# Kernel tuning notes

Measured on AMD Instinct MI355X. Metric: run time of the kernel, lower is better.

## Reference

```python
import jax, jax.numpy as jnp
import numpy as np

B, U, D_DEC, D_ENC = 32, 4096, 512, 512
ATT_UNITS, NUM_HEADS = 512, 4
HEAD_DIM = ATT_UNITS // NUM_HEADS
CONV_FILTERS, CONV_K = 32, 31
INIT = 0.075


def setup_inputs() -> dict:
    key = jax.random.key(0)
    ks = jax.random.split(key, 12)
    u = lambda k, shape: jax.random.uniform(k, shape, jnp.float32, -INIT, INIT)
    return {
        "dec_state": jax.random.normal(ks[0], (B, D_DEC), jnp.float32),
        "enc_state": jax.random.normal(ks[1], (B, U, D_ENC), jnp.float32),
        "prev_attention_weights": jax.random.uniform(ks[2], (B, U), jnp.float32),
        # stacked per-head Dense params
        "Wphi": u(ks[3], (NUM_HEADS, D_DEC, HEAD_DIM)),
        "bphi": jnp.zeros((NUM_HEADS, HEAD_DIM), jnp.float32),
        "Wpsi": u(ks[4], (NUM_HEADS, D_ENC, HEAD_DIM)),
        "bpsi": jnp.zeros((NUM_HEADS, HEAD_DIM), jnp.float32),
        # Conv1D kernel in WIO layout: (kernel_size, in_ch=1, out_ch=32), no bias
        "conv_kernel": jax.random.uniform(ks[5], (CONV_K, 1, CONV_FILTERS), jnp.float32, -0.1, 0.1),
        "Wloc": u(ks[6], (CONV_FILTERS, NUM_HEADS)),
        "Wout": u(ks[7], (NUM_HEADS * D_ENC, ATT_UNITS)),
        "bout": jnp.zeros((ATT_UNITS,), jnp.float32),
    }


def reference(dec_state, enc_state, prev_attention_weights,
              Wphi, bphi, Wpsi, bpsi, conv_kernel, Wloc, Wout, bout):
    # location features: Conv1D(same, no bias) over prev attention weights
    loc_feat = jax.lax.conv_general_dilated(
        prev_attention_weights[:, :, None], conv_kernel,
        window_strides=(1,), padding="SAME",
        dimension_numbers=("NWC", "WIO", "NWC"))            # (B, U, 32)
    loc_bias = loc_feat @ Wloc                                 # (B, U, H)
    loc_bias = jnp.transpose(loc_bias, (0, 2, 1))              # (B, H, U)

    # batched per-head projections (replaces the Python per-head loop)
    phi_s = jnp.einsum("bd,hdk->bhk", dec_state, Wphi) + bphi          # (B, H, hd)
    psi_h = jnp.einsum("bue,hek->bhuk", enc_state, Wpsi) + bpsi[:, None, :]  # (B, H, U, hd)

    energy = jnp.einsum("bhk,bhuk->bhu", phi_s, psi_h) + loc_bias      # (B, H, U)
    attn = jax.nn.softmax(energy, axis=-1)                              # (B, H, U)

    context = jnp.einsum("bhu,bue->bhe", attn, enc_state)               # (B, H, E)
    combined = context.reshape(context.shape[0], -1)                    # (B, H*E)
    context_vector = combined @ Wout + bout                             # (B, ATT_UNITS)
    attention_weights = jnp.mean(attn, axis=1)                          # (B, U)
    return context_vector, attention_weights
```

## Files before the change

kernel.cpp:

```cpp
#include <hip/hip_runtime.h>
#include <math.h>

#define B  32
#define U  4096
#define D  512
#define H  4
#define HD 128
#define CK 31
#define CF 32
#define AU 512

#define WPB    128
#define ROWS_W 32

__global__ __launch_bounds__(256) void prep_kernel(
    const float* __restrict__ dec,
    const float* __restrict__ Wphi,
    const float* __restrict__ bphi,
    const float* __restrict__ Wpsi,
    const float* __restrict__ bpsi,
    const float* __restrict__ convk,
    const float* __restrict__ Wloc,
    float* __restrict__ ws_v,
    float* __restrict__ ws_const,
    float* __restrict__ ws_ck)
{
    __shared__ float decs[D];
    __shared__ float phis[HD];
    const int b = blockIdx.x / H, h = blockIdx.x % H;
    const int tid = threadIdx.x;

    for (int i = tid; i < D; i += 256) decs[i] = dec[b * D + i];
    __syncthreads();

    if (tid < HD) {
        float acc = bphi[h * HD + tid];
        const float* wp = Wphi + (size_t)h * D * HD + tid;
        #pragma unroll 8
        for (int d = 0; d < D; ++d) acc += decs[d] * wp[(size_t)d * HD];
        phis[tid] = acc;
    }
    __syncthreads();

    if (tid == 0) {
        float c = 0.f;
        for (int k = 0; k < HD; ++k) c += phis[k] * bpsi[h * HD + k];
        ws_const[b * H + h] = c;
    }

    for (int e = tid; e < D; e += 256) {
        const float* wq = Wpsi + ((size_t)h * D + e) * HD;
        float acc = 0.f;
        #pragma unroll 8
        for (int k = 0; k < HD; ++k) acc += wq[k] * phis[k];
        ws_v[((size_t)b * H + h) * D + e] = acc;
    }

    if (blockIdx.x == 0 && tid < CK * H) {
        int t = tid / H, hh = tid % H;
        float acc = 0.f;
        for (int f = 0; f < CF; ++f) acc += convk[t * CF + f] * Wloc[f * H + hh];
        ws_ck[t * H + hh] = acc;
    }
}

__global__ __launch_bounds__(256) void fused_pass1(
    const float* __restrict__ enc,
    const float* __restrict__ prevw,
    const float* __restrict__ ws_v,
    const float* __restrict__ ws_const,
    const float* __restrict__ ws_ck,
    float* __restrict__ energy,
    float* __restrict__ pctx,
    float* __restrict__ pms)
{
    const int b    = blockIdx.y;
    const int tid  = threadIdx.x;
    const int lane = tid & 63;
    const int wave = tid >> 6;
    const int widx = blockIdx.x * 4 + wave;
    const int ubase = widx * ROWS_W;

    float4 v0[H], v1[H];
    #pragma unroll
    for (int h = 0; h < H; ++h) {
        const float* vp = ws_v + ((size_t)b * H + h) * D + lane * 8;
        v0[h] = *(const float4*)vp;
        v1[h] = *(const float4*)(vp + 4);
    }
    float ckr[H] = {0.f, 0.f, 0.f, 0.f};
    if (lane < CK) {
        #pragma unroll
        for (int h = 0; h < H; ++h) ckr[h] = ws_ck[lane * H + h];
    }
    float ct[H];
    #pragma unroll
    for (int h = 0; h < H; ++h) ct[h] = ws_const[b * H + h];

    float m0 = -3.402823466e38f, m1 = m0, m2 = m0, m3 = m0;
    float s0 = 0.f, s1 = 0.f, s2 = 0.f, s3 = 0.f;
    float4 z = {0.f, 0.f, 0.f, 0.f};
    float4 c00 = z, c01 = z, c10 = z, c11 = z, c20 = z, c21 = z, c30 = z, c31 = z;

    const bool b16 = (lane & 16) != 0;
    const bool b32 = (lane & 32) != 0;

    const float* encb = enc + ((size_t)b * U + ubase) * D + lane * 8;
    float4 e0 = *(const float4*)encb;
    float4 e1 = *(const float4*)(encb + 4);

    for (int r = 0; r < ROWS_W; ++r) {
        float4 n0, n1;
        if (r < ROWS_W - 1) {
            const float* nx = encb + (size_t)(r + 1) * D;
            n0 = *(const float4*)nx;
            n1 = *(const float4*)(nx + 4);
        }
        const int u = ubase + r;
        float pw = 0.f;
        const int up = u - 15 + lane;
        if (lane < CK && up >= 0 && up < U) pw = prevw[b * U + up];

        float p0 = pw * ckr[0]
            + e0.x*v0[0].x + e0.y*v0[0].y + e0.z*v0[0].z + e0.w*v0[0].w
            + e1.x*v1[0].x + e1.y*v1[0].y + e1.z*v1[0].z + e1.w*v1[0].w;
        float p1 = pw * ckr[1]
            + e0.x*v0[1].x + e0.y*v0[1].y + e0.z*v0[1].z + e0.w*v0[1].w
            + e1.x*v1[1].x + e1.y*v1[1].y + e1.z*v1[1].z + e1.w*v1[1].w;
        float p2 = pw * ckr[2]
            + e0.x*v0[2].x + e0.y*v0[2].y + e0.z*v0[2].z + e0.w*v0[2].w
            + e1.x*v1[2].x + e1.y*v1[2].y + e1.z*v1[2].z + e1.w*v1[2].w;
        float p3 = pw * ckr[3]
            + e0.x*v0[3].x + e0.y*v0[3].y + e0.z*v0[3].z + e0.w*v0[3].w
            + e1.x*v1[3].x + e1.y*v1[3].y + e1.z*v1[3].z + e1.w*v1[3].w;

        float keepA = b16 ? p1 : p0, sendA = b16 ? p0 : p1;
        float a  = keepA + __shfl_xor(sendA, 16);
        float keepB = b16 ? p3 : p2, sendB = b16 ? p2 : p3;
        float bb = keepB + __shfl_xor(sendB, 16);
        float keepC = b32 ? bb : a, sendC = b32 ? a : bb;
        float c = keepC + __shfl_xor(sendC, 32);
        c += __shfl_xor(c, 1);
        c += __shfl_xor(c, 2);
        c += __shfl_xor(c, 4);
        c += __shfl_xor(c, 8);
        float d1 = __shfl_xor(c, 16);
        float d2 = __shfl_xor(c, 32);
        float d3 = __shfl_xor(d1, 32);
        float eh0 = (b32 ? (b16 ? d3 : d2) : (b16 ? d1 : c)) + ct[0];
        float eh1 = (b32 ? (b16 ? d2 : d3) : (b16 ? c  : d1)) + ct[1];
        float eh2 = (b32 ? (b16 ? d1 : c ) : (b16 ? d3 : d2)) + ct[2];
        float eh3 = (b32 ? (b16 ? c  : d1) : (b16 ? d2 : d3)) + ct[3];

        if (lane < H) {
            float ev = (lane == 0) ? eh0 : (lane == 1) ? eh1 : (lane == 2) ? eh2 : eh3;
            energy[((size_t)b * H + lane) * U + u] = ev;
        }

        float mn0 = fmaxf(m0, eh0), mn1 = fmaxf(m1, eh1);
        float mn2 = fmaxf(m2, eh2), mn3 = fmaxf(m3, eh3);
        if (mn0 > m0 || mn1 > m1 || mn2 > m2 || mn3 > m3) {
            float a0 = __expf(m0 - mn0), a1 = __expf(m1 - mn1);
            float a2 = __expf(m2 - mn2), a3 = __expf(m3 - mn3);
            s0 *= a0; s1 *= a1; s2 *= a2; s3 *= a3;
            c00.x*=a0; c00.y*=a0; c00.z*=a0; c00.w*=a0; c01.x*=a0; c01.y*=a0; c01.z*=a0; c01.w*=a0;
            c10.x*=a1; c10.y*=a1; c10.z*=a1; c10.w*=a1; c11.x*=a1; c11.y*=a1; c11.z*=a1; c11.w*=a1;
            c20.x*=a2; c20.y*=a2; c20.z*=a2; c20.w*=a2; c21.x*=a2; c21.y*=a2; c21.z*=a2; c21.w*=a2;
            c30.x*=a3; c30.y*=a3; c30.z*=a3; c30.w*=a3; c31.x*=a3; c31.y*=a3; c31.z*=a3; c31.w*=a3;
            m0 = mn0; m1 = mn1; m2 = mn2; m3 = mn3;
        }
        float w0 = __expf(eh0 - m0), w1 = __expf(eh1 - m1);
        float w2 = __expf(eh2 - m2), w3 = __expf(eh3 - m3);
        s0 += w0; s1 += w1; s2 += w2; s3 += w3;
        c00.x += w0*e0.x; c00.y += w0*e0.y; c00.z += w0*e0.z; c00.w += w0*e0.w;
        c01.x += w0*e1.x; c01.y += w0*e1.y; c01.z += w0*e1.z; c01.w += w0*e1.w;
        c10.x += w1*e0.x; c10.y += w1*e0.y; c10.z += w1*e0.z; c10.w += w1*e0.w;
        c11.x += w1*e1.x; c11.y += w1*e1.y; c11.z += w1*e1.z; c11.w += w1*e1.w;
        c20.x += w2*e0.x; c20.y += w2*e0.y; c20.z += w2*e0.z; c20.w += w2*e0.w;
        c21.x += w2*e1.x; c21.y += w2*e1.y; c21.z += w2*e1.z; c21.w += w2*e1.w;
        c30.x += w3*e0.x; c30.y += w3*e0.y; c30.z += w3*e0.z; c30.w += w3*e0.w;
        c31.x += w3*e1.x; c31.y += w3*e1.y; c31.z += w3*e1.z; c31.w += w3*e1.w;

        e0 = n0; e1 = n1;
    }

    const size_t pbase = ((size_t)(b * WPB + widx)) * H;
    float* p0p = pctx + (pbase + 0) * D + lane * 8;
    float* p1p = pctx + (pbase + 1) * D + lane * 8;
    float* p2p = pctx + (pbase + 2) * D + lane * 8;
    float* p3p = pctx + (pbase + 3) * D + lane * 8;
    *(float4*)p0p = c00; *(float4*)(p0p + 4) = c01;
    *(float4*)p1p = c10; *(float4*)(p1p + 4) = c11;
    *(float4*)p2p = c20; *(float4*)(p2p + 4) = c21;
    *(float4*)p3p = c30; *(float4*)(p3p + 4) = c31;
    if (lane == 0) {
        float* ms = pms + pbase * 2;
        ms[0] = m0; ms[1] = s0; ms[2] = m1; ms[3] = s1;
        ms[4] = m2; ms[5] = s2; ms[6] = m3; ms[7] = s3;
    }
}

__global__ __launch_bounds__(256) void combine_kernel(
    const float* __restrict__ pctx,
    const float* __restrict__ pms,
    float* __restrict__ ctx,
    float* __restrict__ MS)
{
    const int bh = blockIdx.x;
    const int b = bh >> 2, h = bh & 3;
    const int tid = threadIdx.x;
    __shared__ float alpha[WPB];
    __shared__ float red[256];

    float m_i = -3.402823466e38f, s_i = 0.f;
    if (tid < WPB) {
        const float* ms = pms + (((size_t)b * WPB + tid) * H + h) * 2;
        m_i = ms[0]; s_i = ms[1];
    }
    red[tid] = m_i; __syncthreads();
    for (int st = 128; st >= 1; st >>= 1) {
        if (tid < st) red[tid] = fmaxf(red[tid], red[tid + st]);
        __syncthreads();
    }
    const float M = red[0]; __syncthreads();

    float a = (tid < WPB) ? __expf(m_i - M) : 0.f;
    if (tid < WPB) alpha[tid] = a;
    red[tid] = s_i * a; __syncthreads();
    for (int st = 128; st >= 1; st >>= 1) {
        if (tid < st) red[tid] += red[tid + st];
        __syncthreads();
    }
    const float S = red[0];
    if (tid == 0) { MS[bh * 2] = M; MS[bh * 2 + 1] = S; }
    const float invS = 1.0f / S;

    float acc0 = 0.f, acc1 = 0.f;
    const float* base = pctx + ((size_t)b * WPB * H + h) * D;
    for (int i = 0; i < WPB; ++i) {
        float al = alpha[i];
        const float* p = base + (size_t)i * H * D;
        acc0 += al * p[tid];
        acc1 += al * p[tid + 256];
    }
    ctx[(size_t)bh * D + tid]       = acc0 * invS;
    ctx[(size_t)bh * D + tid + 256] = acc1 * invS;
}

__global__ __launch_bounds__(256) void attw_kernel(
    const float* __restrict__ energy,
    const float* __restrict__ MS,
    float* __restrict__ attw)
{
    const int b = blockIdx.x, tid = threadIdx.x;
    float M[H], iS[H];
    #pragma unroll
    for (int h = 0; h < H; ++h) {
        M[h]  = MS[(b * H + h) * 2];
        iS[h] = 1.0f / MS[(b * H + h) * 2 + 1];
    }
    #pragma unroll
    for (int i = 0; i < 16; ++i) {
        const int u = tid + i * 256;
        float acc = 0.f;
        #pragma unroll
        for (int h = 0; h < H; ++h)
            acc += __expf(energy[((size_t)b * H + h) * U + u] - M[h]) * iS[h];
        attw[(size_t)b * U + u] = acc * 0.25f;
    }
}

__global__ __launch_bounds__(256) void outproj_kernel(
    const float* __restrict__ ctx,
    const float* __restrict__ Wout,
    const float* __restrict__ bout,
    float* __restrict__ outv)
{
    const int b = blockIdx.y;
    const int j = blockIdx.x * 256 + threadIdx.x;
    const int i0 = blockIdx.z * 512;
    __shared__ float c_s[512];
    for (int i = threadIdx.x; i < 512; i += 256)
        c_s[i] = ctx[(size_t)b * (H * D) + i0 + i];
    __syncthreads();

    float acc = (blockIdx.z == 0) ? bout[j] : 0.f;
    #pragma unroll 8
    for (int i = 0; i < 512; ++i)
        acc += c_s[i] * Wout[(size_t)(i0 + i) * AU + j];
    atomicAdd(&outv[(size_t)b * AU + j], acc);
}

extern "C" void kernel_launch(void* const* d_in, const int* in_sizes, int n_in,
                              void* d_out, int out_size, void* d_ws, size_t ws_size,
                              hipStream_t stream) {
    const float* dec   = (const float*)d_in[0];
    const float* enc   = (const float*)d_in[1];
    const float* prevw = (const float*)d_in[2];
    const float* Wphi  = (const float*)d_in[3];
    const float* bphi  = (const float*)d_in[4];
    const float* Wpsi  = (const float*)d_in[5];
    const float* bpsi  = (const float*)d_in[6];
    const float* convk = (const float*)d_in[7];
    const float* Wloc  = (const float*)d_in[8];
    const float* Wout  = (const float*)d_in[9];
    const float* bout  = (const float*)d_in[10];

    float* out  = (float*)d_out;
    float* outv = out;
    float* attw = out + B * AU;

    float* ws        = (float*)d_ws;
    float* ws_v      = ws;
    float* ws_const  = ws + 65536;
    float* ws_ck     = ws + 65664;
    float* ws_energy = ws + 65792;
    float* ws_pctx   = ws_energy + (size_t)B*H*U;
    float* ws_pms    = ws_pctx + (size_t)B*WPB*H*D;
    float* ws_MS     = ws_pms + (size_t)B*WPB*H*2;
    float* ws_ctx    = ws_MS + 256;

    hipMemsetAsync(outv, 0, (size_t)B * AU * sizeof(float), stream);

    prep_kernel<<<dim3(B * H), 256, 0, stream>>>(dec, Wphi, bphi, Wpsi, bpsi,
                                                 convk, Wloc, ws_v, ws_const, ws_ck);
    fused_pass1<<<dim3(WPB / 4, B), 256, 0, stream>>>(enc, prevw, ws_v, ws_const,
                                                      ws_ck, ws_energy, ws_pctx, ws_pms);
    combine_kernel<<<dim3(B * H), 256, 0, stream>>>(ws_pctx, ws_pms, ws_ctx, ws_MS);
    attw_kernel<<<dim3(B), 256, 0, stream>>>(ws_energy, ws_MS, attw);
    outproj_kernel<<<dim3(2, B, 4), 256, 0, stream>>>(ws_ctx, Wout, bout, outv);
}
```

Before: 482.3 us.

## Reduce per-wave partial contexts in shared memory before writing to global

The main pass now merges the four waves' online-softmax partial contexts inside each block through shared memory, so it writes one partial per block instead of one per wave. This cuts the partial-context traffic and the combine work by a factor of four, at the cost of 32KB of shared memory per block and extra barriers. The prep kernel also splits the phi projection across all 256 threads, and the output projection uses twice as many z-slices to raise parallelism, which adds more atomics.

```diff
diff --git a/kernel.cpp b/kernel.cpp
--- a/kernel.cpp
+++ b/kernel.cpp
@@ -10,7 +10,7 @@
 #define CF 32
 #define AU 512
 
-#define WPB    128
+#define BPB    32
 #define ROWS_W 32
 
 __global__ __launch_bounds__(256) void prep_kernel(
@@ -26,6 +26,7 @@
     float* __restrict__ ws_ck)
 {
     __shared__ float decs[D];
+    __shared__ float phis2[2][HD];
     __shared__ float phis[HD];
     const int b = blockIdx.x / H, h = blockIdx.x % H;
     const int tid = threadIdx.x;
@@ -33,13 +34,17 @@
     for (int i = tid; i < D; i += 256) decs[i] = dec[b * D + i];
     __syncthreads();
 
-    if (tid < HD) {
-        float acc = bphi[h * HD + tid];
-        const float* wp = Wphi + (size_t)h * D * HD + tid;
+    {
+        const int k = tid & 127, half = tid >> 7;
+        const int d0 = half * 256;
+        float acc = 0.f;
+        const float* wp = Wphi + (size_t)h * D * HD + (size_t)d0 * HD + k;
         #pragma unroll 8
-        for (int d = 0; d < D; ++d) acc += decs[d] * wp[(size_t)d * HD];
-        phis[tid] = acc;
-    }
+        for (int d = 0; d < 256; ++d) acc += decs[d0 + d] * wp[(size_t)d * HD];
+        phis2[half][k] = acc;
+    }
+    __syncthreads();
+    if (tid < HD) phis[tid] = phis2[0][tid] + phis2[1][tid] + bphi[h * HD + tid];
     __syncthreads();
 
     if (tid == 0) {
@@ -75,11 +80,15 @@
     float* __restrict__ pms)
 {
     const int b    = blockIdx.y;
+    const int blk  = blockIdx.x;
     const int tid  = threadIdx.x;
     const int lane = tid & 63;
     const int wave = tid >> 6;
-    const int widx = blockIdx.x * 4 + wave;
-    const int ubase = widx * ROWS_W;
+    const int ubase = (blk * 4 + wave) * ROWS_W;
+
+    __shared__ float lctx[4][H][D];
+    __shared__ float lms[4][H][2];
+    __shared__ float lalpha[H][4];
 
     float4 v0[H], v1[H];
     #pragma unroll
@@ -184,19 +193,50 @@
         e0 = n0; e1 = n1;
     }
 
-    const size_t pbase = ((size_t)(b * WPB + widx)) * H;
-    float* p0p = pctx + (pbase + 0) * D + lane * 8;
-    float* p1p = pctx + (pbase + 1) * D + lane * 8;
-    float* p2p = pctx + (pbase + 2) * D + lane * 8;
-    float* p3p = pctx + (pbase + 3) * D + lane * 8;
-    *(float4*)p0p = c00; *(float4*)(p0p + 4) = c01;
-    *(float4*)p1p = c10; *(float4*)(p1p + 4) = c11;
-    *(float4*)p2p = c20; *(float4*)(p2p + 4) = c21;
-    *(float4*)p3p = c30; *(float4*)(p3p + 4) = c31;
+    *(float4*)&lctx[wave][0][lane * 8]     = c00;
+    *(float4*)&lctx[wave][0][lane * 8 + 4] = c01;
+    *(float4*)&lctx[wave][1][lane * 8]     = c10;
+    *(float4*)&lctx[wave][1][lane * 8 + 4] = c11;
+    *(float4*)&lctx[wave][2][lane * 8]     = c20;
+    *(float4*)&lctx[wave][2][lane * 8 + 4] = c21;
+    *(float4*)&lctx[wave][3][lane * 8]     = c30;
+    *(float4*)&lctx[wave][3][lane * 8 + 4] = c31;
     if (lane == 0) {
-        float* ms = pms + pbase * 2;
-        ms[0] = m0; ms[1] = s0; ms[2] = m1; ms[3] = s1;
-        ms[4] = m2; ms[5] = s2; ms[6] = m3; ms[7] = s3;
+        lms[wave][0][0] = m0; lms[wave][0][1] = s0;
+        lms[wave][1][0] = m1; lms[wave][1][1] = s1;
+        lms[wave][2][0] = m2; lms[wave][2][1] = s2;
+        lms[wave][3][0] = m3; lms[wave][3][1] = s3;
+    }
+    __syncthreads();
+
+    const size_t pbase = ((size_t)(b * BPB + blk)) * H;
+    if (tid < H) {
+        const int h = tid;
+        float M = fmaxf(fmaxf(lms[0][h][0], lms[1][h][0]),
+                        fmaxf(lms[2][h][0], lms[3][h][0]));
+        float S = 0.f;
+        #pragma unroll
+        for (int w = 0; w < 4; ++w) {
+            float al = __expf(lms[w][h][0] - M);
+            lalpha[h][w] = al;
+            S += al * lms[w][h][1];
+        }
+        pms[(pbase + h) * 2]     = M;
+        pms[(pbase + h) * 2 + 1] = S;
+    }
+    __syncthreads();
+
+    #pragma unroll
+    for (int h = 0; h < H; ++h) {
+        const float a0 = lalpha[h][0], a1 = lalpha[h][1];
+        const float a2 = lalpha[h][2], a3 = lalpha[h][3];
+        #pragma unroll
+        for (int half = 0; half < 2; ++half) {
+            const int d = tid + half * 256;
+            float val = a0 * lctx[0][h][d] + a1 * lctx[1][h][d]
+                      + a2 * lctx[2][h][d] + a3 * lctx[3][h][d];
+            pctx[(pbase + h) * D + d] = val;
+        }
     }
 }
 
@@ -209,36 +249,34 @@
     const int bh = blockIdx.x;
     const int b = bh >> 2, h = bh & 3;
     const int tid = threadIdx.x;
-    __shared__ float alpha[WPB];
-    __shared__ float red[256];
-
-    float m_i = -3.402823466e38f, s_i = 0.f;
-    if (tid < WPB) {
-        const float* ms = pms + (((size_t)b * WPB + tid) * H + h) * 2;
-        m_i = ms[0]; s_i = ms[1];
-    }
-    red[tid] = m_i; __syncthreads();
-    for (int st = 128; st >= 1; st >>= 1) {
-        if (tid < st) red[tid] = fmaxf(red[tid], red[tid + st]);
-        __syncthreads();
-    }
-    const float M = red[0]; __syncthreads();
-
-    float a = (tid < WPB) ? __expf(m_i - M) : 0.f;
-    if (tid < WPB) alpha[tid] = a;
-    red[tid] = s_i * a; __syncthreads();
-    for (int st = 128; st >= 1; st >>= 1) {
-        if (tid < st) red[tid] += red[tid + st];
-        __syncthreads();
-    }
-    const float S = red[0];
-    if (tid == 0) { MS[bh * 2] = M; MS[bh * 2 + 1] = S; }
-    const float invS = 1.0f / S;
+    __shared__ float sm[BPB], ss[BPB], salpha[BPB];
+    __shared__ float MSsh[2];
+
+    if (tid < BPB) {
+        sm[tid] = pms[(((size_t)b * BPB + tid) * H + h) * 2];
+        ss[tid] = pms[(((size_t)b * BPB + tid) * H + h) * 2 + 1];
+    }
+    __syncthreads();
+    if (tid == 0) {
+        float M = -3.402823466e38f;
+        for (int i = 0; i < BPB; ++i) M = fmaxf(M, sm[i]);
+        float S = 0.f;
+        for (int i = 0; i < BPB; ++i) {
+            float al = __expf(sm[i] - M);
+            salpha[i] = al;
+            S += al * ss[i];
+        }
+        MSsh[0] = M; MSsh[1] = S;
+        MS[bh * 2] = M; MS[bh * 2 + 1] = S;
+    }
+    __syncthreads();
+    const float invS = 1.0f / MSsh[1];
 
     float acc0 = 0.f, acc1 = 0.f;
-    const float* base = pctx + ((size_t)b * WPB * H + h) * D;
-    for (int i = 0; i < WPB; ++i) {
-        float al = alpha[i];
+    const float* base = pctx + ((size_t)b * BPB * H + h) * D;
+    #pragma unroll 4
+    for (int i = 0; i < BPB; ++i) {
+        float al = salpha[i];
         const float* p = base + (size_t)i * H * D;
         acc0 += al * p[tid];
         acc1 += al * p[tid + 256];
@@ -278,15 +316,14 @@
 {
     const int b = blockIdx.y;
     const int j = blockIdx.x * 256 + threadIdx.x;
-    const int i0 = blockIdx.z * 512;
-    __shared__ float c_s[512];
-    for (int i = threadIdx.x; i < 512; i += 256)
-        c_s[i] = ctx[(size_t)b * (H * D) + i0 + i];
+    const int i0 = blockIdx.z * 256;
+    __shared__ float c_s[256];
+    c_s[threadIdx.x] = ctx[(size_t)b * (H * D) + i0 + threadIdx.x];
     __syncthreads();
 
     float acc = (blockIdx.z == 0) ? bout[j] : 0.f;
     #pragma unroll 8
-    for (int i = 0; i < 512; ++i)
+    for (int i = 0; i < 256; ++i)
         acc += c_s[i] * Wout[(size_t)(i0 + i) * AU + j];
     atomicAdd(&outv[(size_t)b * AU + j], acc);
 }
@@ -316,17 +353,17 @@
     float* ws_ck     = ws + 65664;
     float* ws_energy = ws + 65792;
     float* ws_pctx   = ws_energy + (size_t)B*H*U;
-    float* ws_pms    = ws_pctx + (size_t)B*WPB*H*D;
-    float* ws_MS     = ws_pms + (size_t)B*WPB*H*2;
+    float* ws_pms    = ws_pctx + (size_t)B*BPB*H*D;
+    float* ws_MS     = ws_pms + (size_t)B*BPB*H*2;
     float* ws_ctx    = ws_MS + 256;
 
     hipMemsetAsync(outv, 0, (size_t)B * AU * sizeof(float), stream);
 
     prep_kernel<<<dim3(B * H), 256, 0, stream>>>(dec, Wphi, bphi, Wpsi, bpsi,
                                                  convk, Wloc, ws_v, ws_const, ws_ck);
-    fused_pass1<<<dim3(WPB / 4, B), 256, 0, stream>>>(enc, prevw, ws_v, ws_const,
-                                                      ws_ck, ws_energy, ws_pctx, ws_pms);
+    fused_pass1<<<dim3(BPB, B), 256, 0, stream>>>(enc, prevw, ws_v, ws_const,
+                                                  ws_ck, ws_energy, ws_pctx, ws_pms);
     combine_kernel<<<dim3(B * H), 256, 0, stream>>>(ws_pctx, ws_pms, ws_ctx, ws_MS);
     attw_kernel<<<dim3(B), 256, 0, stream>>>(ws_energy, ws_MS, attw);
-    outproj_kernel<<<dim3(2, B, 4), 256, 0, stream>>>(ws_ctx, Wout, bout, outv);
-}
+    outproj_kernel<<<dim3(2, B, 8), 256, 0, stream>>>(ws_ctx, Wout, bout, outv);
+}
```

After: 448.3 us. 7.0% less time.
